# Performance work log

Hardware: AMD Instinct MI355X
Metric: run time of the kernel (lower is better)

The kernel has to match this reference:

```python
import jax, jax.numpy as jnp
import numpy as np

N_NODES = 100000
N_EDGES = 600000
D_IN = 128
D_HID = 128
D_OUT = 128


def setup_inputs() -> dict:
    key = jax.random.key(0)
    k = jax.random.split(key, 6)
    x = jax.random.normal(k[0], (N_NODES, D_IN), dtype=jnp.float32)
    edge_index = jax.random.randint(k[1], (2, N_EDGES), 0, N_NODES, dtype=jnp.int64)
    # GCNConv params: glorot-ish weights, zero-init biases (randn-scaled here)
    W1 = jax.random.normal(k[2], (D_IN, D_HID), dtype=jnp.float32) / np.sqrt(D_IN)
    b1 = jnp.zeros((D_HID,), dtype=jnp.float32)
    W2 = jax.random.normal(k[3], (D_HID, D_OUT), dtype=jnp.float32) / np.sqrt(D_HID)
    b2 = jnp.zeros((D_OUT,), dtype=jnp.float32)
    return {"x": x, "edge_index": edge_index, "W1": W1, "b1": b1, "W2": W2, "b2": b2}


def _gcn_conv(x, W, b, src, dst, deg_inv_sqrt, n_nodes):
    # PyG GCNConv: h = x @ W; out_i = sum_{j->i} d_j^{-1/2} d_i^{-1/2} h_j + b
    h = x @ W  # [N, Dout]
    norm = (deg_inv_sqrt[src] * deg_inv_sqrt[dst])[:, None]  # [E, 1]
    msg = h[src] * norm  # gather: [E, Dout]
    out = jax.ops.segment_sum(msg, dst, num_segments=n_nodes)  # scatter-add
    return out + b


def reference(x, edge_index, W1, b1, W2, b2):
    n = x.shape[0]
    # add self loops
    loops = jnp.arange(n, dtype=edge_index.dtype)
    src = jnp.concatenate([edge_index[0], loops])
    dst = jnp.concatenate([edge_index[1], loops])
    # symmetric normalization degrees (computed on dst, deg >= 1 due to self loops)
    deg = jax.ops.segment_sum(jnp.ones_like(dst, dtype=x.dtype), dst, num_segments=n)
    deg_inv_sqrt = jax.lax.rsqrt(deg)
    h = _gcn_conv(x, W1, b1, src, dst, deg_inv_sqrt, n)
    h = jax.nn.relu(h)  # dropout is identity in eval mode
    out = _gcn_conv(h, W2, b2, src, dst, deg_inv_sqrt, n)
    return out
```

## Files before the change

kernel.cpp:

```cpp
#include <hip/hip_runtime.h>

#define D 128

typedef __attribute__((ext_vector_type(8))) short bf16x8;
typedef __attribute__((ext_vector_type(4))) float f32x4;
typedef __attribute__((ext_vector_type(4))) unsigned u32x4;

__device__ inline unsigned short f2bf(float f) {
    unsigned u = __builtin_bit_cast(unsigned, f);
    u += 0x7FFFu + ((u >> 16) & 1u);
    return (unsigned short)(u >> 16);
}
__device__ inline float bf_lo(unsigned u) { return __builtin_bit_cast(float, u << 16); }
__device__ inline float bf_hi(unsigned u) { return __builtin_bit_cast(float, u & 0xFFFF0000u); }

__global__ __launch_bounds__(256) void k_pack_zero(const float* __restrict__ W1,
                                                   const float* __restrict__ W2,
                                                   unsigned short* __restrict__ wp,
                                                   int* __restrict__ counts, int n) {
    if (blockIdx.x < 16) {
        const int t = blockIdx.x * 256 + threadIdx.x;
        const float* W = (t < 2048) ? W1 : W2;
        const int tt = t & 2047;
        const int lane = tt & 63;
        const int frag = tt >> 6;
        const int ct = frag >> 2;
        const int kk = frag & 3;
        const int col16 = lane & 15;
        const int kgrp = lane >> 4;
        bf16x8 d;
#pragma unroll
        for (int e = 0; e < 8; ++e)
            d[e] = (short)f2bf(W[(kk * 32 + kgrp * 8 + e) * D + ct * 16 + col16]);
        *reinterpret_cast<bf16x8*>(wp + (size_t)t * 8) = d;
    } else {
        const int i = (blockIdx.x - 16) * 256 + threadIdx.x;
        if (i < n) counts[i] = 0;
    }
}

__global__ void k_hist_rank(const int* __restrict__ dst, int* __restrict__ counts,
                            int* __restrict__ rank, int nE) {
    int e4 = (blockIdx.x * blockDim.x + threadIdx.x) * 4;
    if (e4 + 4 <= nE) {
        const int4 d = *reinterpret_cast<const int4*>(dst + e4);
        int4 r;
        r.x = atomicAdd(&counts[d.x], 1);
        r.y = atomicAdd(&counts[d.y], 1);
        r.z = atomicAdd(&counts[d.z], 1);
        r.w = atomicAdd(&counts[d.w], 1);
        *reinterpret_cast<int4*>(rank + e4) = r;
    } else {
        for (int e = e4; e < nE; ++e) rank[e] = atomicAdd(&counts[dst[e]], 1);
    }
}

__global__ __launch_bounds__(256) void k_scan_part(const int* __restrict__ counts,
                                                   int* __restrict__ bsum,
                                                   float* __restrict__ dis, int n) {
    const int t = threadIdx.x;
    const int base = blockIdx.x * 1024 + t * 4;
    int4 c = make_int4(0, 0, 0, 0);
    if (base + 4 <= n) {
        c = *reinterpret_cast<const int4*>(counts + base);
        float4 dv;
        dv.x = rsqrtf((float)(c.x + 1));
        dv.y = rsqrtf((float)(c.y + 1));
        dv.z = rsqrtf((float)(c.z + 1));
        dv.w = rsqrtf((float)(c.w + 1));
        *reinterpret_cast<float4*>(dis + base) = dv;
    } else if (base < n) {
        int cc[4] = {0, 0, 0, 0};
        for (int k = 0; k < 4; ++k)
            if (base + k < n) {
                cc[k] = counts[base + k];
                dis[base + k] = rsqrtf((float)(cc[k] + 1));
            }
        c.x = cc[0]; c.y = cc[1]; c.z = cc[2]; c.w = cc[3];
    }
    __shared__ int red[256];
    red[t] = c.x + c.y + c.z + c.w;
    __syncthreads();
    for (int off = 128; off > 0; off >>= 1) {
        if (t < off) red[t] += red[t + off];
        __syncthreads();
    }
    if (t == 0) bsum[blockIdx.x] = red[0];
}

__global__ __launch_bounds__(256) void k_scan_final(const int* __restrict__ counts,
                                                    const int* __restrict__ bsum,
                                                    int* __restrict__ starts, int n, int nB) {
    __shared__ int sb[128];
    __shared__ int ts[256];
    const int t = threadIdx.x;
    const int b = blockIdx.x;

    if (t < 128) sb[t] = (t < nB) ? bsum[t] : 0;
    __syncthreads();
    for (int off = 1; off < 128; off <<= 1) {
        int add = (t < 128 && t >= off) ? sb[t - off] : 0;
        __syncthreads();
        if (t < 128) sb[t] += add;
        __syncthreads();
    }
    const int block_off = (b > 0) ? sb[b - 1] : 0;

    const int base = b * 1024 + t * 4;
    int4 c = make_int4(0, 0, 0, 0);
    if (base + 4 <= n) {
        c = *reinterpret_cast<const int4*>(counts + base);
    } else if (base < n) {
        if (base + 0 < n) c.x = counts[base + 0];
        if (base + 1 < n) c.y = counts[base + 1];
        if (base + 2 < n) c.z = counts[base + 2];
    }
    const int s = c.x + c.y + c.z + c.w;
    ts[t] = s;
    __syncthreads();
    for (int off = 1; off < 256; off <<= 1) {
        int add = (t >= off) ? ts[t - off] : 0;
        __syncthreads();
        ts[t] += add;
        __syncthreads();
    }
    int excl = block_off + ts[t] - s;

    int4 w;
    w.x = excl;
    w.y = w.x + c.x;
    w.z = w.y + c.y;
    w.w = w.z + c.z;
    if (base + 4 <= n) {
        *reinterpret_cast<int4*>(starts + base) = w;
    } else if (base < n) {
        if (base + 0 < n) starts[base + 0] = w.x;
        if (base + 1 < n) starts[base + 1] = w.y;
        if (base + 2 < n) starts[base + 2] = w.z;
    }
    if (b == 0 && t == 0) starts[n] = sb[nB - 1];
}

__global__ void k_scatter_nr(const int* __restrict__ src, const int* __restrict__ dst,
                             const int* __restrict__ rank, const int* __restrict__ starts,
                             int* __restrict__ esrc, int nE) {
    int e4 = (blockIdx.x * blockDim.x + threadIdx.x) * 4;
    if (e4 + 4 <= nE) {
        const int4 s = *reinterpret_cast<const int4*>(src + e4);
        const int4 d = *reinterpret_cast<const int4*>(dst + e4);
        const int4 r = *reinterpret_cast<const int4*>(rank + e4);
        esrc[starts[d.x] + r.x] = s.x;
        esrc[starts[d.y] + r.y] = s.y;
        esrc[starts[d.z] + r.z] = s.z;
        esrc[starts[d.w] + r.w] = s.w;
    } else {
        for (int e = e4; e < nE; ++e)
            esrc[starts[dst[e]] + rank[e]] = src[e];
    }
}

__device__ __forceinline__ void accum_chunk(const unsigned short* __restrict__ hs,
                                            int myedge, int cnt, int grp, int sub,
                                            float acc[8]) {
    auto row16 = [&](int s) -> u32x4 {
        return *reinterpret_cast<const u32x4*>(hs + (size_t)s * D + sub * 8);
    };
    for (int k = 0; k < cnt; k += 8) {
        u32x4 u[8];
#pragma unroll
        for (int q = 0; q < 8; ++q) {
            const int tq = min(k + q, cnt - 1);
            const int s = __shfl(myedge, (grp << 4) | tq);
            u[q] = row16(s);
        }
        const int rem = cnt - k;
#pragma unroll
        for (int q = 0; q < 8; ++q) {
            if (q < rem) {
#pragma unroll
                for (int e = 0; e < 4; ++e) {
                    acc[2 * e] += bf_lo(u[q][e]);
                    acc[2 * e + 1] += bf_hi(u[q][e]);
                }
            }
        }
    }
}

template <bool IN_BF16, bool RELU>
__global__ __launch_bounds__(256, 3) void k_gemm_mfma(const void* __restrict__ Xv,
                                                      const unsigned short* __restrict__ wp,
                                                      const float* __restrict__ dis,
                                                      unsigned short* __restrict__ outbf,
                                                      int n) {
    __shared__ __align__(16) unsigned short At[64 * 128];
    const int tid = threadIdx.x;
    const int lane = tid & 63;
    const int wv = tid >> 6;
    const int col16 = lane & 15;
    const int kgrp = lane >> 4;
    const int st = blockIdx.x;

    float4 pf[8];
    bf16x8 pb[4];
#pragma unroll
    for (int c = 0; c < 4; ++c) {
        const int idx = c * 2048 + tid * 8;
        const int row = idx >> 7;
        const int col = idx & 127;
        int grow = st * 64 + row;
        if (grow >= n) grow = n - 1;
        if constexpr (IN_BF16) {
            pb[c] = *reinterpret_cast<const bf16x8*>(
                    (const unsigned short*)Xv + (size_t)grow * D + col);
        } else {
            const float4* p = reinterpret_cast<const float4*>(
                    (const float*)Xv + (size_t)grow * D + col);
            pf[2 * c] = p[0];
            pf[2 * c + 1] = p[1];
        }
    }

#pragma unroll
    for (int c = 0; c < 4; ++c) {
        const int idx = c * 2048 + tid * 8;
        const int row = idx >> 7;
        const int col = idx & 127;
        bf16x8 d;
        if constexpr (IN_BF16) {
            d = pb[c];
            if (RELU) {
#pragma unroll
                for (int e = 0; e < 8; ++e)
                    d[e] = (short)((d[e] & (short)0x8000) ? 0 : d[e]);
            }
        } else {
            const float4 f0 = pf[2 * c], f1 = pf[2 * c + 1];
            float v[8] = {f0.x, f0.y, f0.z, f0.w, f1.x, f1.y, f1.z, f1.w};
#pragma unroll
            for (int e = 0; e < 8; ++e) {
                float f = v[e];
                if (RELU) f = fmaxf(f, 0.0f);
                d[e] = (short)f2bf(f);
            }
        }
        const int waddr = row * 128 + (col ^ ((row & 7) << 3));
        *reinterpret_cast<bf16x8*>(&At[waddr]) = d;
    }
    __syncthreads();

    bf16x8 a[4];
#pragma unroll
    for (int kk = 0; kk < 4; ++kk) {
        const int raddr = (wv * 16 + col16) * 128 +
                          ((kk * 32 + kgrp * 8) ^ ((col16 & 7) << 3));
        a[kk] = *reinterpret_cast<const bf16x8*>(&At[raddr]);
    }

    const int node = st * 64 + wv * 16 + col16;
    const float dn = (node < n) ? dis[node] : 0.0f;
    unsigned short* op = outbf + (size_t)node * D + kgrp * 4;

#pragma unroll
    for (int h = 0; h < 2; ++h) {
        bf16x8 bw[4][4];
#pragma unroll
        for (int c2 = 0; c2 < 4; ++c2)
#pragma unroll
            for (int kk = 0; kk < 4; ++kk)
                bw[c2][kk] = *reinterpret_cast<const bf16x8*>(
                        wp + (size_t)(((h * 4 + c2) * 4 + kk) * 64 + lane) * 8);

        f32x4 acc[4];
#pragma unroll
        for (int c2 = 0; c2 < 4; ++c2) acc[c2] = (f32x4){0.f, 0.f, 0.f, 0.f};
#pragma unroll
        for (int kk = 0; kk < 4; ++kk)
#pragma unroll
            for (int c2 = 0; c2 < 4; ++c2)
                acc[c2] = __builtin_amdgcn_mfma_f32_16x16x32_bf16(bw[c2][kk], a[kk], acc[c2], 0, 0, 0);

        if (node < n) {
#pragma unroll
            for (int c2 = 0; c2 < 4; ++c2) {
                uint2 w;
                w.x = (unsigned)f2bf(dn * acc[c2][0]) | ((unsigned)f2bf(dn * acc[c2][1]) << 16);
                w.y = (unsigned)f2bf(dn * acc[c2][2]) | ((unsigned)f2bf(dn * acc[c2][3]) << 16);
                *reinterpret_cast<uint2*>(op + (h * 4 + c2) * 16) = w;
            }
        }
    }
}

__global__ __launch_bounds__(256, 3) void k_gather_gemm(const unsigned short* __restrict__ hs,
                                                        const int* __restrict__ starts,
                                                        const int* __restrict__ esrc,
                                                        const float* __restrict__ dis,
                                                        const float* __restrict__ bias,
                                                        const unsigned short* __restrict__ wp,
                                                        unsigned short* __restrict__ outbf,
                                                        int n) {
    __shared__ __align__(16) unsigned short At[64 * 128];
    const int tid = threadIdx.x;
    const int lane = tid & 63;
    const int wv = tid >> 6;
    const int col16 = lane & 15;
    const int kgrp = lane >> 4;
    const int grp = lane >> 4;
    const int sub = lane & 15;
    const int st = blockIdx.x;

    const float4 bv0 = reinterpret_cast<const float4*>(bias)[sub * 2 + 0];
    const float4 bv1 = reinterpret_cast<const float4*>(bias)[sub * 2 + 1];

    int ic[4], beg[4], end[4], cnt0[4], my[4];
    float di[4];
    u32x4 selfrow[4];
#pragma unroll
    for (int p = 0; p < 4; ++p) {
        const int i = st * 64 + wv * 16 + p * 4 + grp;
        ic[p] = (i < n) ? i : (n - 1);
    }
#pragma unroll
    for (int p = 0; p < 4; ++p) {
        beg[p] = starts[ic[p]];
        end[p] = starts[ic[p] + 1];
        di[p] = dis[ic[p]];
        selfrow[p] = *reinterpret_cast<const u32x4*>(hs + (size_t)ic[p] * D + sub * 8);
    }
#pragma unroll
    for (int p = 0; p < 4; ++p) {
        cnt0[p] = min(end[p] - beg[p], 16);
        my[p] = (sub < cnt0[p]) ? esrc[beg[p] + sub] : 0;
    }

#pragma unroll
    for (int p = 0; p < 4; ++p) {
        float acc[8];
#pragma unroll
        for (int e = 0; e < 4; ++e) {
            acc[2 * e] = bf_lo(selfrow[p][e]);
            acc[2 * e + 1] = bf_hi(selfrow[p][e]);
        }
        if (cnt0[p] > 0) accum_chunk(hs, my[p], cnt0[p], grp, sub, acc);
        for (int j = beg[p] + 16; j < end[p]; j += 16) {
            const int cnt = min(end[p] - j, 16);
            const int me = (sub < cnt) ? esrc[j + sub] : 0;
            accum_chunk(hs, me, cnt, grp, sub, acc);
        }

        float o[8];
        o[0] = di[p] * acc[0] + bv0.x; o[1] = di[p] * acc[1] + bv0.y;
        o[2] = di[p] * acc[2] + bv0.z; o[3] = di[p] * acc[3] + bv0.w;
        o[4] = di[p] * acc[4] + bv1.x; o[5] = di[p] * acc[5] + bv1.y;
        o[6] = di[p] * acc[6] + bv1.z; o[7] = di[p] * acc[7] + bv1.w;

        u32x4 w;
#pragma unroll
        for (int e = 0; e < 4; ++e)
            w[e] = (unsigned)f2bf(fmaxf(o[2 * e], 0.0f)) |
                   ((unsigned)f2bf(fmaxf(o[2 * e + 1], 0.0f)) << 16);
        const int lrow = wv * 16 + p * 4 + grp;
        const int waddr = lrow * 128 + ((sub * 8) ^ ((lrow & 7) << 3));
        *reinterpret_cast<u32x4*>(&At[waddr]) = w;
    }
    __syncthreads();

    bf16x8 a[4];
#pragma unroll
    for (int kk = 0; kk < 4; ++kk) {
        const int raddr = (wv * 16 + col16) * 128 +
                          ((kk * 32 + kgrp * 8) ^ ((col16 & 7) << 3));
        a[kk] = *reinterpret_cast<const bf16x8*>(&At[raddr]);
    }

    const int node = st * 64 + wv * 16 + col16;
    const float dn = (node < n) ? dis[node] : 0.0f;
    unsigned short* op = outbf + (size_t)node * D + kgrp * 4;

#pragma unroll
    for (int h = 0; h < 2; ++h) {
        bf16x8 bw[4][4];
#pragma unroll
        for (int c2 = 0; c2 < 4; ++c2)
#pragma unroll
            for (int kk = 0; kk < 4; ++kk)
                bw[c2][kk] = *reinterpret_cast<const bf16x8*>(
                        wp + (size_t)(((h * 4 + c2) * 4 + kk) * 64 + lane) * 8);

        f32x4 acc[4];
#pragma unroll
        for (int c2 = 0; c2 < 4; ++c2) acc[c2] = (f32x4){0.f, 0.f, 0.f, 0.f};
#pragma unroll
        for (int kk = 0; kk < 4; ++kk)
#pragma unroll
            for (int c2 = 0; c2 < 4; ++c2)
                acc[c2] = __builtin_amdgcn_mfma_f32_16x16x32_bf16(bw[c2][kk], a[kk], acc[c2], 0, 0, 0);

        if (node < n) {
#pragma unroll
            for (int c2 = 0; c2 < 4; ++c2) {
                uint2 w;
                w.x = (unsigned)f2bf(dn * acc[c2][0]) | ((unsigned)f2bf(dn * acc[c2][1]) << 16);
                w.y = (unsigned)f2bf(dn * acc[c2][2]) | ((unsigned)f2bf(dn * acc[c2][3]) << 16);
                *reinterpret_cast<uint2*>(op + (h * 4 + c2) * 16) = w;
            }
        }
    }
}

__global__ __launch_bounds__(256) void k_gather_agg(const unsigned short* __restrict__ hs,
                                                    const int* __restrict__ starts,
                                                    const int* __restrict__ esrc,
                                                    const float* __restrict__ dis,
                                                    const float* __restrict__ b,
                                                    float* __restrict__ outv, int n) {
    const int lane = threadIdx.x & 63;
    const int wv = threadIdx.x >> 6;
    const int grp = lane >> 4;
    const int sub = lane & 15;
    const int i = (blockIdx.x * 4 + wv) * 4 + grp;
    const bool active = (i < n);
    const int ic = active ? i : (n - 1);

    const float di = dis[ic];
    const int beg = starts[ic];
    const int end = starts[ic + 1];

    float acc[8];
    {
        const u32x4 u = *reinterpret_cast<const u32x4*>(hs + (size_t)ic * D + sub * 8);
#pragma unroll
        for (int e = 0; e < 4; ++e) {
            acc[2 * e] = bf_lo(u[e]);
            acc[2 * e + 1] = bf_hi(u[e]);
        }
    }
    for (int j = beg; j < end; j += 16) {
        const int cnt = min(end - j, 16);
        const int me = (sub < cnt) ? esrc[j + sub] : 0;
        accum_chunk(hs, me, cnt, grp, sub, acc);
    }

    if (!active) return;

    const float4 bv0 = reinterpret_cast<const float4*>(b)[sub * 2 + 0];
    const float4 bv1 = reinterpret_cast<const float4*>(b)[sub * 2 + 1];
    float4* op = reinterpret_cast<float4*>(outv + (size_t)i * D + sub * 8);
    op[0] = make_float4(di * acc[0] + bv0.x, di * acc[1] + bv0.y,
                        di * acc[2] + bv0.z, di * acc[3] + bv0.w);
    op[1] = make_float4(di * acc[4] + bv1.x, di * acc[5] + bv1.y,
                        di * acc[6] + bv1.z, di * acc[7] + bv1.w);
}

extern "C" void kernel_launch(void* const* d_in, const int* in_sizes, int n_in,
                              void* d_out, int out_size, void* d_ws, size_t ws_size,
                              hipStream_t stream) {
    const float* x  = (const float*)d_in[0];
    const int*   ei = (const int*)d_in[1];
    const float* W1 = (const float*)d_in[2];
    const float* b1 = (const float*)d_in[3];
    const float* W2 = (const float*)d_in[4];
    const float* b2 = (const float*)d_in[5];
    float* out = (float*)d_out;

    const int n  = in_sizes[0] / D;
    const int nE = in_sizes[1] / 2;
    const int* src = ei;
    const int* dst = ei + nE;

    char* ws = (char*)d_ws;
    float*          dis    = (float*)(ws);
    int*            counts = (int*)(ws + (1ull  << 19));
    int*            starts = (int*)(ws + (2ull  << 19));
    int*            esrc   = (int*)(ws + (4ull  << 19));
    int*            bsum   = (int*)(ws + (6ull  << 20));
    unsigned short* hs_bf  = (unsigned short*)(ws + (8ull  << 20));
    int*            rank   = (int*)(ws + (34ull << 20));
    unsigned short* wp     = (unsigned short*)(ws + (37ull << 20));
    unsigned short* hs2_bf = (unsigned short*)(ws + (40ull << 20));

    unsigned short* wp1 = wp;
    unsigned short* wp2 = wp + 2048 * 8;

    const int B = 256;
    const int gn = (n + B - 1) / B;
    const int ge4 = (nE + B * 4 - 1) / (B * 4);
    const int nB = (n + 1023) / 1024;

    k_pack_zero<<<16 + gn, B, 0, stream>>>(W1, W2, wp, counts, n);

    k_hist_rank<<<ge4, B, 0, stream>>>(dst, counts, rank, nE);
    k_scan_part<<<nB, B, 0, stream>>>(counts, bsum, dis, n);
    k_scan_final<<<nB, B, 0, stream>>>(counts, bsum, starts, n, nB);
    k_scatter_nr<<<ge4, B, 0, stream>>>(src, dst, rank, starts, esrc, nE);

    const int nst = (n + 63) / 64;
    const int agg_grid = (n + 15) / 16;

    k_gemm_mfma<false, false><<<nst, B, 0, stream>>>(x, wp1, dis, hs_bf, n);
    k_gather_gemm<<<nst, B, 0, stream>>>(hs_bf, starts, esrc, dis, b1, wp2, hs2_bf, n);
    k_gather_agg<<<agg_grid, B, 0, stream>>>(hs2_bf, starts, esrc, dis, b2, out, n);
}
```

Baseline: 144.8 us.

## Merge edge scatter into first GEMM launch and interleave gather across four nodes

Fuses the CSR edge-scatter kernel and the first-layer MFMA GEMM into one launch, with block-index ranges selecting the role, so the two independent stages run concurrently and one launch is removed. In the gather-GEMM kernel, the first chunk of neighbor rows for all four nodes a wave handles is now loaded together in groups of four, which puts more memory loads in flight. The cost is higher register pressure from the 4x8 accumulators and 16 outstanding row loads, plus LDS reserved by the scatter blocks that never use it.

```diff
diff --git a/kernel.cpp b/kernel.cpp
--- a/kernel.cpp
+++ b/kernel.cpp
@@ -141,21 +141,107 @@
     if (b == 0 && t == 0) starts[n] = sb[nB - 1];
 }
 
-__global__ void k_scatter_nr(const int* __restrict__ src, const int* __restrict__ dst,
-                             const int* __restrict__ rank, const int* __restrict__ starts,
-                             int* __restrict__ esrc, int nE) {
-    int e4 = (blockIdx.x * blockDim.x + threadIdx.x) * 4;
-    if (e4 + 4 <= nE) {
-        const int4 s = *reinterpret_cast<const int4*>(src + e4);
-        const int4 d = *reinterpret_cast<const int4*>(dst + e4);
-        const int4 r = *reinterpret_cast<const int4*>(rank + e4);
-        esrc[starts[d.x] + r.x] = s.x;
-        esrc[starts[d.y] + r.y] = s.y;
-        esrc[starts[d.z] + r.z] = s.z;
-        esrc[starts[d.w] + r.w] = s.w;
-    } else {
-        for (int e = e4; e < nE; ++e)
-            esrc[starts[dst[e]] + rank[e]] = src[e];
+__global__ __launch_bounds__(256, 3) void k_scatter_gemm(const int* __restrict__ src,
+                                                         const int* __restrict__ dst,
+                                                         const int* __restrict__ rank,
+                                                         const int* __restrict__ starts,
+                                                         int* __restrict__ esrc, int nE, int nsc,
+                                                         const float* __restrict__ X,
+                                                         const unsigned short* __restrict__ wp,
+                                                         const float* __restrict__ dis,
+                                                         unsigned short* __restrict__ outbf,
+                                                         int n) {
+    __shared__ __align__(16) unsigned short At[64 * 128];
+    if (blockIdx.x < nsc) {
+        int e4 = (blockIdx.x * blockDim.x + threadIdx.x) * 4;
+        if (e4 + 4 <= nE) {
+            const int4 s = *reinterpret_cast<const int4*>(src + e4);
+            const int4 d = *reinterpret_cast<const int4*>(dst + e4);
+            const int4 r = *reinterpret_cast<const int4*>(rank + e4);
+            esrc[starts[d.x] + r.x] = s.x;
+            esrc[starts[d.y] + r.y] = s.y;
+            esrc[starts[d.z] + r.z] = s.z;
+            esrc[starts[d.w] + r.w] = s.w;
+        } else {
+            for (int e = e4; e < nE; ++e)
+                esrc[starts[dst[e]] + rank[e]] = src[e];
+        }
+        return;
+    }
+    const int st = blockIdx.x - nsc;
+    const int tid = threadIdx.x;
+    const int lane = tid & 63;
+    const int wv = tid >> 6;
+    const int col16 = lane & 15;
+    const int kgrp = lane >> 4;
+
+    float4 pf[8];
+#pragma unroll
+    for (int c = 0; c < 4; ++c) {
+        const int idx = c * 2048 + tid * 8;
+        const int row = idx >> 7;
+        const int col = idx & 127;
+        int grow = st * 64 + row;
+        if (grow >= n) grow = n - 1;
+        const float4* p = reinterpret_cast<const float4*>(X + (size_t)grow * D + col);
+        pf[2 * c] = p[0];
+        pf[2 * c + 1] = p[1];
+    }
+#pragma unroll
+    for (int c = 0; c < 4; ++c) {
+        const int idx = c * 2048 + tid * 8;
+        const int row = idx >> 7;
+        const int col = idx & 127;
+        const float4 f0 = pf[2 * c], f1 = pf[2 * c + 1];
+        float v[8] = {f0.x, f0.y, f0.z, f0.w, f1.x, f1.y, f1.z, f1.w};
+        bf16x8 d;
+#pragma unroll
+        for (int e = 0; e < 8; ++e) d[e] = (short)f2bf(v[e]);
+        const int waddr = row * 128 + (col ^ ((row & 7) << 3));
+        *reinterpret_cast<bf16x8*>(&At[waddr]) = d;
+    }
+    __syncthreads();
+
+    bf16x8 a[4];
+#pragma unroll
+    for (int kk = 0; kk < 4; ++kk) {
+        const int raddr = (wv * 16 + col16) * 128 +
+                          ((kk * 32 + kgrp * 8) ^ ((col16 & 7) << 3));
+        a[kk] = *reinterpret_cast<const bf16x8*>(&At[raddr]);
+    }
+
+    const int node = st * 64 + wv * 16 + col16;
+    const float dn = (node < n) ? dis[node] : 0.0f;
+    unsigned short* op = outbf + (size_t)node * D + kgrp * 4;
+
+#pragma unroll
+    for (int h = 0; h < 2; ++h) {
+        bf16x8 bw[4][4];
+#pragma unroll
+        for (int c2 = 0; c2 < 4; ++c2)
+#pragma unroll
+            for (int kk = 0; kk < 4; ++kk)
+                bw[c2][kk] = *reinterpret_cast<const bf16x8*>(
+                        wp + (size_t)(((h * 4 + c2) * 4 + kk) * 64 + lane) * 8);
+
+        f32x4 acc[4];
+#pragma unroll
+        for (int c2 = 0; c2 < 4; ++c2) acc[c2] = (f32x4){0.f, 0.f, 0.f, 0.f};
+#pragma unroll
+        for (int kk = 0; kk < 4; ++kk)
+#pragma unroll
+            for (int c2 = 0; c2 < 4; ++c2)
+                acc[c2] = __builtin_amdgcn_mfma_f32_16x16x32_bf16(bw[c2][kk], a[kk], acc[c2], 0, 0, 0);
+
+        if (node < n) {
+#pragma unroll
+            for (int c2 = 0; c2 < 4; ++c2) {
+                uint2 w;
+                w.x = (unsigned)f2bf(dn * acc[c2][0]) | ((unsigned)f2bf(dn * acc[c2][1]) << 16);
+                w.y = (unsigned)f2bf(dn * acc[c2][2]) | ((unsigned)f2bf(dn * acc[c2][3]) << 16);
+                *reinterpret_cast<uint2*>(op + (h * 4 + c2) * 16) = w;
+            }
+        }
     }
 }
 
@@ -182,111 +268,6 @@
                     acc[2 * e] += bf_lo(u[q][e]);
                     acc[2 * e + 1] += bf_hi(u[q][e]);
                 }
-            }
-        }
-    }
-}
-
-template <bool IN_BF16, bool RELU>
-__global__ __launch_bounds__(256, 3) void k_gemm_mfma(const void* __restrict__ Xv,
-                                                      const unsigned short* __restrict__ wp,
-                                                      const float* __restrict__ dis,
-                                                      unsigned short* __restrict__ outbf,
-                                                      int n) {
-    __shared__ __align__(16) unsigned short At[64 * 128];
-    const int tid = threadIdx.x;
-    const int lane = tid & 63;
-    const int wv = tid >> 6;
-    const int col16 = lane & 15;
-    const int kgrp = lane >> 4;
-    const int st = blockIdx.x;
-
-    float4 pf[8];
-    bf16x8 pb[4];
-#pragma unroll
-    for (int c = 0; c < 4; ++c) {
-        const int idx = c * 2048 + tid * 8;
-        const int row = idx >> 7;
-        const int col = idx & 127;
-        int grow = st * 64 + row;
-        if (grow >= n) grow = n - 1;
-        if constexpr (IN_BF16) {
-            pb[c] = *reinterpret_cast<const bf16x8*>(
-                    (const unsigned short*)Xv + (size_t)grow * D + col);
-        } else {
-            const float4* p = reinterpret_cast<const float4*>(
-                    (const float*)Xv + (size_t)grow * D + col);
-            pf[2 * c] = p[0];
-            pf[2 * c + 1] = p[1];
-        }
-    }
-
-#pragma unroll
-    for (int c = 0; c < 4; ++c) {
-        const int idx = c * 2048 + tid * 8;
-        const int row = idx >> 7;
-        const int col = idx & 127;
-        bf16x8 d;
-        if constexpr (IN_BF16) {
-            d = pb[c];
-            if (RELU) {
-#pragma unroll
-                for (int e = 0; e < 8; ++e)
-                    d[e] = (short)((d[e] & (short)0x8000) ? 0 : d[e]);
-            }
-        } else {
-            const float4 f0 = pf[2 * c], f1 = pf[2 * c + 1];
-            float v[8] = {f0.x, f0.y, f0.z, f0.w, f1.x, f1.y, f1.z, f1.w};
-#pragma unroll
-            for (int e = 0; e < 8; ++e) {
-                float f = v[e];
-                if (RELU) f = fmaxf(f, 0.0f);
-                d[e] = (short)f2bf(f);
-            }
-        }
-        const int waddr = row * 128 + (col ^ ((row & 7) << 3));
-        *reinterpret_cast<bf16x8*>(&At[waddr]) = d;
-    }
-    __syncthreads();
-
-    bf16x8 a[4];
-#pragma unroll
-    for (int kk = 0; kk < 4; ++kk) {
-        const int raddr = (wv * 16 + col16) * 128 +
-                          ((kk * 32 + kgrp * 8) ^ ((col16 & 7) << 3));
-        a[kk] = *reinterpret_cast<const bf16x8*>(&At[raddr]);
-    }
-
-    const int node = st * 64 + wv * 16 + col16;
-    const float dn = (node < n) ? dis[node] : 0.0f;
-    unsigned short* op = outbf + (size_t)node * D + kgrp * 4;
-
-#pragma unroll
-    for (int h = 0; h < 2; ++h) {
-        bf16x8 bw[4][4];
-#pragma unroll
-        for (int c2 = 0; c2 < 4; ++c2)
-#pragma unroll
-            for (int kk = 0; kk < 4; ++kk)
-                bw[c2][kk] = *reinterpret_cast<const bf16x8*>(
-                        wp + (size_t)(((h * 4 + c2) * 4 + kk) * 64 + lane) * 8);
-
-        f32x4 acc[4];
-#pragma unroll
-        for (int c2 = 0; c2 < 4; ++c2) acc[c2] = (f32x4){0.f, 0.f, 0.f, 0.f};
-#pragma unroll
-        for (int kk = 0; kk < 4; ++kk)
-#pragma unroll
-            for (int c2 = 0; c2 < 4; ++c2)
-                acc[c2] = __builtin_amdgcn_mfma_f32_16x16x32_bf16(bw[c2][kk], a[kk], acc[c2], 0, 0, 0);
-
-        if (node < n) {
-#pragma unroll
-            for (int c2 = 0; c2 < 4; ++c2) {
-                uint2 w;
-                w.x = (unsigned)f2bf(dn * acc[c2][0]) | ((unsigned)f2bf(dn * acc[c2][1]) << 16);
-                w.y = (unsigned)f2bf(dn * acc[c2][2]) | ((unsigned)f2bf(dn * acc[c2][3]) << 16);
-                *reinterpret_cast<uint2*>(op + (h * 4 + c2) * 16) = w;
             }
         }
     }
@@ -313,6 +294,10 @@
     const float4 bv0 = reinterpret_cast<const float4*>(bias)[sub * 2 + 0];
     const float4 bv1 = reinterpret_cast<const float4*>(bias)[sub * 2 + 1];
 
+    auto row16 = [&](int s) -> u32x4 {
+        return *reinterpret_cast<const u32x4*>(hs + (size_t)s * D + sub * 8);
+    };
+
     int ic[4], beg[4], end[4], cnt0[4], my[4];
     float di[4];
     u32x4 selfrow[4];
@@ -326,7 +311,7 @@
         beg[p] = starts[ic[p]];
         end[p] = starts[ic[p] + 1];
         di[p] = dis[ic[p]];
-        selfrow[p] = *reinterpret_cast<const u32x4*>(hs + (size_t)ic[p] * D + sub * 8);
+        selfrow[p] = row16(ic[p]);
     }
 #pragma unroll
     for (int p = 0; p < 4; ++p) {
@@ -334,26 +319,56 @@
         my[p] = (sub < cnt0[p]) ? esrc[beg[p] + sub] : 0;
     }
 
-#pragma unroll
-    for (int p = 0; p < 4; ++p) {
-        float acc[8];
+    float acc[4][8];
+#pragma unroll
+    for (int p = 0; p < 4; ++p)
 #pragma unroll
         for (int e = 0; e < 4; ++e) {
-            acc[2 * e] = bf_lo(selfrow[p][e]);
-            acc[2 * e + 1] = bf_hi(selfrow[p][e]);
-        }
-        if (cnt0[p] > 0) accum_chunk(hs, my[p], cnt0[p], grp, sub, acc);
+            acc[p][2 * e] = bf_lo(selfrow[p][e]);
+            acc[p][2 * e + 1] = bf_hi(selfrow[p][e]);
+        }
+
+    const int mx = max(max(cnt0[0], cnt0[1]), max(cnt0[2], cnt0[3]));
+    for (int k = 0; k < mx; k += 4) {
+        u32x4 u[4][4];
+#pragma unroll
+        for (int p = 0; p < 4; ++p)
+#pragma unroll
+            for (int q = 0; q < 4; ++q) {
+                const int tq = max(min(k + q, cnt0[p] - 1), 0);
+                const int s = __shfl(my[p], (grp << 4) | tq);
+                u[p][q] = row16(s);
+            }
+#pragma unroll
+        for (int p = 0; p < 4; ++p) {
+            const int rem = cnt0[p] - k;
+#pragma unroll
+            for (int q = 0; q < 4; ++q) {
+                if (q < rem) {
+#pragma unroll
+                    for (int e = 0; e < 4; ++e) {
+                        acc[p][2 * e] += bf_lo(u[p][q][e]);
+                        acc[p][2 * e + 1] += bf_hi(u[p][q][e]);
+                    }
+                }
+            }
+        }
+    }
+#pragma unroll
+    for (int p = 0; p < 4; ++p)
         for (int j = beg[p] + 16; j < end[p]; j += 16) {
             const int cnt = min(end[p] - j, 16);
             const int me = (sub < cnt) ? esrc[j + sub] : 0;
-            accum_chunk(hs, me, cnt, grp, sub, acc);
-        }
-
+            accum_chunk(hs, me, cnt, grp, sub, acc[p]);
+        }
+
+#pragma unroll
+    for (int p = 0; p < 4; ++p) {
         float o[8];
-        o[0] = di[p] * acc[0] + bv0.x; o[1] = di[p] * acc[1] + bv0.y;
-        o[2] = di[p] * acc[2] + bv0.z; o[3] = di[p] * acc[3] + bv0.w;
-        o[4] = di[p] * acc[4] + bv1.x; o[5] = di[p] * acc[5] + bv1.y;
-        o[6] = di[p] * acc[6] + bv1.z; o[7] = di[p] * acc[7] + bv1.w;
+        o[0] = di[p] * acc[p][0] + bv0.x; o[1] = di[p] * acc[p][1] + bv0.y;
+        o[2] = di[p] * acc[p][2] + bv0.z; o[3] = di[p] * acc[p][3] + bv0.w;
+        o[4] = di[p] * acc[p][4] + bv1.x; o[5] = di[p] * acc[p][5] + bv1.y;
+        o[6] = di[p] * acc[p][6] + bv1.z; o[7] = di[p] * acc[p][7] + bv1.w;
 
         u32x4 w;
 #pragma unroll
@@ -388,21 +403,21 @@
                 bw[c2][kk] = *reinterpret_cast<const bf16x8*>(
                         wp + (size_t)(((h * 4 + c2) * 4 + kk) * 64 + lane) * 8);
 
-        f32x4 acc[4];
-#pragma unroll
-        for (int c2 = 0; c2 < 4; ++c2) acc[c2] = (f32x4){0.f, 0.f, 0.f, 0.f};
+        f32x4 acc2[4];
+#pragma unroll
+        for (int c2 = 0; c2 < 4; ++c2) acc2[c2] = (f32x4){0.f, 0.f, 0.f, 0.f};
 #pragma unroll
         for (int kk = 0; kk < 4; ++kk)
 #pragma unroll
             for (int c2 = 0; c2 < 4; ++c2)
-                acc[c2] = __builtin_amdgcn_mfma_f32_16x16x32_bf16(bw[c2][kk], a[kk], acc[c2], 0, 0, 0);
+                acc2[c2] = __builtin_amdgcn_mfma_f32_16x16x32_bf16(bw[c2][kk], a[kk], acc2[c2], 0, 0, 0);
 
         if (node < n) {
 #pragma unroll
             for (int c2 = 0; c2 < 4; ++c2) {
                 uint2 w;
-                w.x = (unsigned)f2bf(dn * acc[c2][0]) | ((unsigned)f2bf(dn * acc[c2][1]) << 16);
-                w.y = (unsigned)f2bf(dn * acc[c2][2]) | ((unsigned)f2bf(dn * acc[c2][3]) << 16);
+                w.x = (unsigned)f2bf(dn * acc2[c2][0]) | ((unsigned)f2bf(dn * acc2[c2][1]) << 16);
+                w.y = (unsigned)f2bf(dn * acc2[c2][2]) | ((unsigned)f2bf(dn * acc2[c2][3]) << 16);
                 *reinterpret_cast<uint2*>(op + (h * 4 + c2) * 16) = w;
             }
         }
@@ -493,12 +508,12 @@
     k_hist_rank<<<ge4, B, 0, stream>>>(dst, counts, rank, nE);
     k_scan_part<<<nB, B, 0, stream>>>(counts, bsum, dis, n);
     k_scan_final<<<nB, B, 0, stream>>>(counts, bsum, starts, n, nB);
-    k_scatter_nr<<<ge4, B, 0, stream>>>(src, dst, rank, starts, esrc, nE);
 
     const int nst = (n + 63) / 64;
     const int agg_grid = (n + 15) / 16;
 
-    k_gemm_mfma<false, false><<<nst, B, 0, stream>>>(x, wp1, dis, hs_bf, n);
+    k_scatter_gemm<<<ge4 + nst, B, 0, stream>>>(src, dst, rank, starts, esrc, nE, ge4,
+                                                x, wp1, dis, hs_bf, n);
     k_gather_gemm<<<nst, B, 0, stream>>>(hs_bf, starts, esrc, dis, b1, wp2, hs2_bf, n);
     k_gather_agg<<<agg_grid, B, 0, stream>>>(hs2_bf, starts, esrc, dis, b2, out, n);
 }
```

Measured after the change: 147.1 us. No clear change (+1.6%).
